# Optimization experiments

Measured on AMD Instinct MI355X. Metric: run time of the kernel, lower is better.

Reference implementation:

```python
import jax, jax.numpy as jnp
import numpy as np

N = 50000      # nodes
E = 800000     # edges
F_IN = 5       # (E, X, Y, Z, T_rel)
D = 128        # hidden_dim
H = 4          # heads
C = D // H     # per-head channels = 32
L = 3          # num_gat_layers
NEG_SLOPE = 0.2


def setup_inputs() -> dict:
    key = jax.random.key(0)
    ks = jax.random.split(key, 20)
    s = 0.05
    inp = {
        "x": jax.random.normal(ks[0], (N, F_IN), dtype=jnp.float32),
        "edge_index": jax.random.randint(ks[1], (2, E), 0, N, dtype=jnp.int32),
        # node encoder
        "enc_W": jax.random.normal(ks[2], (F_IN, D), dtype=jnp.float32) * s,
        "enc_b": jnp.zeros((D,), jnp.float32),
        # stacked GATv2 params for L layers
        "Wl": jax.random.normal(ks[3], (L, D, D), dtype=jnp.float32) * s,
        "bl": jnp.zeros((L, D), jnp.float32),
        "Wr": jax.random.normal(ks[4], (L, D, D), dtype=jnp.float32) * s,
        "br": jnp.zeros((L, D), jnp.float32),
        "att": jax.random.normal(ks[5], (L, H, C), dtype=jnp.float32) * s,
        "gat_bias": jnp.zeros((L, D), jnp.float32),
        # edge classifier MLP (258 -> 128 -> 64 -> 1)
        "c1_W": jax.random.normal(ks[6], (2 * D + 2, D), dtype=jnp.float32) * s,
        "c1_b": jnp.zeros((D,), jnp.float32),
        "c2_W": jax.random.normal(ks[7], (D, 64), dtype=jnp.float32) * s,
        "c2_b": jnp.zeros((64,), jnp.float32),
        "c3_W": jax.random.normal(ks[8], (64, 1), dtype=jnp.float32) * s,
        "c3_b": jnp.zeros((1,), jnp.float32),
    }
    return inp


def _gatv2_layer(h, src, dst, Wl, bl, Wr, br, att, bias):
    # GATv2Conv (PyG semantics, share_weights=False, concat=True, self-loops added)
    xl = (h @ Wl + bl).reshape(N, H, C)   # source transform
    xr = (h @ Wr + br).reshape(N, H, C)   # target transform
    e = jax.nn.leaky_relu(xl[src] + xr[dst], NEG_SLOPE)      # [E', H, C]
    alpha = jnp.einsum("ehc,hc->eh", e, att)                 # [E', H]
    # scatter-softmax over incoming edges of each dst node (numerically stable)
    amax = jax.ops.segment_max(alpha, dst, num_segments=N)
    alpha = jnp.exp(alpha - amax[dst])
    denom = jax.ops.segment_sum(alpha, dst, num_segments=N)
    alpha = alpha / (denom[dst] + 1e-16)
    msg = xl[src] * alpha[:, :, None]                        # [E', H, C]
    out = jax.ops.segment_sum(msg, dst, num_segments=N)      # [N, H, C]
    return out.reshape(N, D) + bias


def reference(x, edge_index, enc_W, enc_b, Wl, bl, Wr, br, att, gat_bias,
              c1_W, c1_b, c2_W, c2_b, c3_W, c3_b):
    h = jax.nn.relu(x @ enc_W + enc_b)
    # add self-loops (PyG GATv2Conv default add_self_loops=True)
    loops = jnp.arange(N, dtype=edge_index.dtype)
    src = jnp.concatenate([edge_index[0], loops])
    dst = jnp.concatenate([edge_index[1], loops])
    for i in range(L):
        h = jax.nn.elu(_gatv2_layer(h, src, dst, Wl[i], bl[i], Wr[i], br[i], att[i], gat_bias[i]))
    # edge feature head on ORIGINAL edges
    row, col = edge_index[0], edge_index[1]
    ni = h[row]                                              # [E, D]
    nj = h[col]                                              # [E, D]
    delta_t = jnp.abs(x[row, 4] - x[col, 4])[:, None]        # [E, 1]
    dist = jnp.sqrt(jnp.sum((x[row, 1:4] - x[col, 1:4]) ** 2, axis=1))[:, None]
    ef = jnp.concatenate([ni, nj, delta_t, dist], axis=1)    # [E, 2D+2]
    o = jax.nn.relu(ef @ c1_W + c1_b)
    o = jax.nn.relu(o @ c2_W + c2_b)
    o = o @ c3_W + c3_b
    return o.reshape(-1)
```

## Files before the change

kernel.cpp:

```cpp
#include <hip/hip_runtime.h>
#include <hip/hip_bf16.h>

#define N_NODES 50000
#define N_EDGES 800000
#define DIM 128
#define NLAYER 3
#define NEG 0.2f

typedef __attribute__((ext_vector_type(8))) short short8;
typedef __attribute__((ext_vector_type(4))) float f32x4;

__global__ __launch_bounds__(256) void zero_kernel(int* p, int n) {
    int i = blockIdx.x * 256 + threadIdx.x;
    if (i < n) p[i] = 0;
}

__global__ __launch_bounds__(256) void hist_kernel(const int* __restrict__ dst, int* __restrict__ counts) {
    int e = blockIdx.x * 256 + threadIdx.x;
    if (e < N_EDGES) atomicAdd(&counts[dst[e]], 1);
}

__global__ __launch_bounds__(256) void scan1_kernel(const int* __restrict__ counts, int* __restrict__ indptr,
                                                    int* __restrict__ bsum, int n) {
    __shared__ int buf[256];
    int t = threadIdx.x;
    int i = blockIdx.x * 256 + t;
    int v = (i < n) ? counts[i] : 0;
    buf[t] = v;
    __syncthreads();
    for (int off = 1; off < 256; off <<= 1) {
        int add = (t >= off) ? buf[t - off] : 0;
        __syncthreads();
        buf[t] += add;
        __syncthreads();
    }
    if (i < n) indptr[i + 1] = buf[t];
    if (t == 255) bsum[blockIdx.x] = buf[255];
}

__global__ __launch_bounds__(256) void scan2_kernel(int* __restrict__ bsum, int* __restrict__ boff,
                                                    int* __restrict__ indptr, int nb) {
    __shared__ int buf[256];
    int t = threadIdx.x;
    int v = (t < nb) ? bsum[t] : 0;
    buf[t] = v;
    __syncthreads();
    for (int off = 1; off < 256; off <<= 1) {
        int add = (t >= off) ? buf[t - off] : 0;
        __syncthreads();
        buf[t] += add;
        __syncthreads();
    }
    if (t < nb) boff[t] = buf[t] - v;
    if (t == 0) indptr[0] = 0;
}

__global__ __launch_bounds__(256) void scan3_kernel(int* __restrict__ indptr, const int* __restrict__ boff, int n) {
    int i = blockIdx.x * 256 + threadIdx.x;
    if (i < n) indptr[i + 1] += boff[i >> 8];
}

__global__ __launch_bounds__(256) void place_kernel(const int* __restrict__ srcp, const int* __restrict__ dstp,
                                                    const int* __restrict__ indptr, int* __restrict__ cursor,
                                                    int* __restrict__ csr_src, int* __restrict__ csr_dst,
                                                    int* __restrict__ csr_eid) {
    int e = blockIdx.x * 256 + threadIdx.x;
    if (e < N_EDGES) {
        int dn = dstp[e];
        int pos = indptr[dn] + atomicAdd(&cursor[dn], 1);
        csr_src[pos] = srcp[e];
        csr_dst[pos] = dn;
        csr_eid[pos] = e;
    }
}

__global__ __launch_bounds__(256) void encoder_kernel(const float* __restrict__ x, const float* __restrict__ W,
                                                      const float* __restrict__ b, float* __restrict__ h) {
    int gid = blockIdx.x * 256 + threadIdx.x;
    int n = gid >> 7, d = gid & 127;
    if (n >= N_NODES) return;
    float acc = b[d];
#pragma unroll
    for (int f = 0; f < 5; f++) acc += x[n * 5 + f] * W[f * DIM + d];
    h[n * DIM + d] = fmaxf(acc, 0.f);
}

__global__ __launch_bounds__(256) void prep_weights_kernel(const float* __restrict__ Wl, const float* __restrict__ Wr,
                                                           const float* __restrict__ c1W,
                                                           unsigned short* __restrict__ wt) {
    int idx = blockIdx.x * 256 + threadIdx.x;
    int m = idx >> 14;
    int r = idx & 16383;
    int n = r >> 7, k = r & 127;
    int L = m >> 1, half = m & 1;
    const float* W;
    if (L < 3) W = (half ? Wr : Wl) + (size_t)L * 16384;
    else W = c1W + (size_t)half * 16384;
    float v = W[k * 128 + n];
    __hip_bfloat16 hb = __float2bfloat16(v);
    float rl = v - __bfloat162float(hb);
    __hip_bfloat16 lb = __float2bfloat16(rl);
    wt[(size_t)m * 32768 + n * 128 + k] = *reinterpret_cast<unsigned short*>(&hb);
    wt[(size_t)m * 32768 + 16384 + n * 128 + k] = *reinterpret_cast<unsigned short*>(&lb);
}

template <bool BF16OUT>
__global__ __launch_bounds__(256) void transform_mfma_kernel(const float* __restrict__ h,
                                                             const unsigned short* __restrict__ wtA,
                                                             const float* __restrict__ bA,
                                                             const unsigned short* __restrict__ wtB,
                                                             const float* __restrict__ bB,
                                                             void* __restrict__ outA_, void* __restrict__ outB_) {
    __shared__ __align__(16) char hhi[64 * 256];
    __shared__ __align__(16) char hlo[64 * 256];
    int t = threadIdx.x;
    int l = t & 63, w = t >> 6;
    int n0 = blockIdx.x * 64;
    for (int i = t; i < 64 * 32; i += 256) {
        int row = i >> 5, c4 = (i & 31) * 4;
        int n = n0 + row;
        float4 v = make_float4(0.f, 0.f, 0.f, 0.f);
        if (n < N_NODES) v = *(const float4*)&h[(size_t)n * DIM + c4];
        const float* pv = &v.x;
        unsigned short hi4[4], lo4[4];
#pragma unroll
        for (int q = 0; q < 4; q++) {
            __hip_bfloat16 hb = __float2bfloat16(pv[q]);
            float rl = pv[q] - __bfloat162float(hb);
            __hip_bfloat16 lb = __float2bfloat16(rl);
            hi4[q] = *reinterpret_cast<unsigned short*>(&hb);
            lo4[q] = *reinterpret_cast<unsigned short*>(&lb);
        }
        int addr = (row * 256 + c4 * 2) ^ ((row & 7) << 4);
        *(ushort4*)(hhi + addr) = make_ushort4(hi4[0], hi4[1], hi4[2], hi4[3]);
        *(ushort4*)(hlo + addr) = make_ushort4(lo4[0], lo4[1], lo4[2], lo4[3]);
    }
    __syncthreads();

    int lane_m = l & 15, lane_k8 = l >> 4;

#pragma unroll
    for (int mat = 0; mat < 2; mat++) {
        const short* wthi = (const short*)(mat ? wtB : wtA);
        const short* wtlo = wthi + 16384;
        const float* bias = mat ? bB : bA;
        short8 bh[2][4], bl_[2][4];
#pragma unroll
        for (int j = 0; j < 2; j++) {
            int nrow = (w * 2 + j) * 16 + lane_m;
#pragma unroll
            for (int ks = 0; ks < 4; ks++) {
                int ke = ks * 32 + lane_k8 * 8;
                bh[j][ks] = *(const short8*)(wthi + nrow * 128 + ke);
                bl_[j][ks] = *(const short8*)(wtlo + nrow * 128 + ke);
            }
        }
        f32x4 acc[4][2];
#pragma unroll
        for (int mt = 0; mt < 4; mt++)
#pragma unroll
            for (int j = 0; j < 2; j++) acc[mt][j] = (f32x4){0.f, 0.f, 0.f, 0.f};
#pragma unroll
        for (int ks = 0; ks < 4; ks++) {
            int kb = ks * 64 + lane_k8 * 16;
#pragma unroll
            for (int mt = 0; mt < 4; mt++) {
                int arow = mt * 16 + lane_m;
                int aswz = (arow & 7) << 4;
                short8 ahi = *(const short8*)(hhi + ((arow * 256 + kb) ^ aswz));
                short8 alo = *(const short8*)(hlo + ((arow * 256 + kb) ^ aswz));
#pragma unroll
                for (int j = 0; j < 2; j++) {
                    acc[mt][j] = __builtin_amdgcn_mfma_f32_16x16x32_bf16(ahi, bh[j][ks], acc[mt][j], 0, 0, 0);
                    acc[mt][j] = __builtin_amdgcn_mfma_f32_16x16x32_bf16(ahi, bl_[j][ks], acc[mt][j], 0, 0, 0);
                    acc[mt][j] = __builtin_amdgcn_mfma_f32_16x16x32_bf16(alo, bh[j][ks], acc[mt][j], 0, 0, 0);
                }
            }
        }
        void* outp = mat ? outB_ : outA_;
#pragma unroll
        for (int j = 0; j < 2; j++) {
            int col = (w * 2 + j) * 16 + lane_m;
            float bv = bias ? bias[col] : 0.f;
#pragma unroll
            for (int mt = 0; mt < 4; mt++) {
#pragma unroll
                for (int r = 0; r < 4; r++) {
                    int node = n0 + mt * 16 + lane_k8 * 4 + r;
                    if (node < N_NODES) {
                        float v = acc[mt][j][r] + bv;
                        if constexpr (BF16OUT) {
                            ((__hip_bfloat16*)outp)[(size_t)node * DIM + col] = __float2bfloat16(v);
                        } else {
                            ((float*)outp)[(size_t)node * DIM + col] = v;
                        }
                    }
                }
            }
        }
    }
}

__global__ __launch_bounds__(256) void gat_edge_kernel(const float* __restrict__ xl, const float* __restrict__ xr,
                                                       const float* __restrict__ att, const float* __restrict__ gbias,
                                                       const int* __restrict__ indptr, const int* __restrict__ csr_src,
                                                       float* __restrict__ h_out) {
    int n = blockIdx.x * 4 + (threadIdx.x >> 6);
    int l = threadIdx.x & 63;
    int half = l >> 5;
    int c0 = (l & 31) * 4;
    float4 xrv = *(const float4*)&xr[(size_t)n * DIM + c0];
    float4 attv = *(const float4*)&att[c0];
    int beg = indptr[n], end = indptr[n + 1];

    float m[4], den[4];
    float4 acc[4];
    {
        float4 v = *(const float4*)&xl[(size_t)n * DIM + c0];
        float z, a;
        z = v.x + xrv.x; z = fmaxf(z, NEG * z); a = z * attv.x;
        z = v.y + xrv.y; z = fmaxf(z, NEG * z); a += z * attv.y;
        z = v.z + xrv.z; z = fmaxf(z, NEG * z); a += z * attv.z;
        z = v.w + xrv.w; z = fmaxf(z, NEG * z); a += z * attv.w;
        a += __shfl_xor(a, 1);
        a += __shfl_xor(a, 2);
        a += __shfl_xor(a, 4);
        if (half == 0) {
            m[0] = a; den[0] = 1.f; acc[0] = v;
        } else {
            m[0] = -3.4e38f; den[0] = 0.f; acc[0] = make_float4(0.f, 0.f, 0.f, 0.f);
        }
#pragma unroll
        for (int c = 1; c < 4; c++) { m[c] = -3.4e38f; den[c] = 0.f; acc[c] = make_float4(0.f, 0.f, 0.f, 0.f); }
    }

    for (int i = beg; i < end; i += 8) {
        int s[4];
        bool val[4];
        float4 v[4];
        float a[4];
#pragma unroll
        for (int c = 0; c < 4; c++) {
            int idx = i + 2 * c + half;
            val[c] = idx < end;
            s[c] = val[c] ? csr_src[idx] : n;
        }
#pragma unroll
        for (int c = 0; c < 4; c++) v[c] = *(const float4*)&xl[(size_t)s[c] * DIM + c0];
#pragma unroll
        for (int c = 0; c < 4; c++) {
            float z, aa;
            z = v[c].x + xrv.x; z = fmaxf(z, NEG * z); aa = z * attv.x;
            z = v[c].y + xrv.y; z = fmaxf(z, NEG * z); aa += z * attv.y;
            z = v[c].z + xrv.z; z = fmaxf(z, NEG * z); aa += z * attv.z;
            z = v[c].w + xrv.w; z = fmaxf(z, NEG * z); aa += z * attv.w;
            a[c] = aa;
        }
#pragma unroll
        for (int off = 1; off <= 4; off <<= 1)
#pragma unroll
            for (int c = 0; c < 4; c++) a[c] += __shfl_xor(a[c], off);
#pragma unroll
        for (int c = 0; c < 4; c++) {
            if (!val[c]) a[c] = -3.4e38f;
            float mn = fmaxf(m[c], a[c]);
            float sc = __expf(m[c] - mn), p = __expf(a[c] - mn);
            den[c] = den[c] * sc + p;
            acc[c].x = acc[c].x * sc + p * v[c].x;
            acc[c].y = acc[c].y * sc + p * v[c].y;
            acc[c].z = acc[c].z * sc + p * v[c].z;
            acc[c].w = acc[c].w * sc + p * v[c].w;
            m[c] = mn;
        }
    }
#pragma unroll
    for (int c = 1; c < 4; c++) {
        float mm = fmaxf(m[0], m[c]);
        float s0 = __expf(m[0] - mm), s1 = __expf(m[c] - mm);
        den[0] = den[0] * s0 + den[c] * s1;
        acc[0].x = acc[0].x * s0 + acc[c].x * s1;
        acc[0].y = acc[0].y * s0 + acc[c].y * s1;
        acc[0].z = acc[0].z * s0 + acc[c].z * s1;
        acc[0].w = acc[0].w * s0 + acc[c].w * s1;
        m[0] = mm;
    }
    {
        float mo = __shfl_xor(m[0], 32);
        float dno = __shfl_xor(den[0], 32);
        float4 ao;
        ao.x = __shfl_xor(acc[0].x, 32);
        ao.y = __shfl_xor(acc[0].y, 32);
        ao.z = __shfl_xor(acc[0].z, 32);
        ao.w = __shfl_xor(acc[0].w, 32);
        float mm = fmaxf(m[0], mo);
        float s0 = __expf(m[0] - mm), s1 = __expf(mo - mm);
        den[0] = den[0] * s0 + dno * s1;
        acc[0].x = acc[0].x * s0 + ao.x * s1;
        acc[0].y = acc[0].y * s0 + ao.y * s1;
        acc[0].z = acc[0].z * s0 + ao.z * s1;
        acc[0].w = acc[0].w * s0 + ao.w * s1;
    }
    if (half == 0) {
        float4 gb = *(const float4*)&gbias[c0];
        float inv = 1.f / (den[0] + 1e-16f);
        float4 o;
        o.x = acc[0].x * inv + gb.x;
        o.y = acc[0].y * inv + gb.y;
        o.z = acc[0].z * inv + gb.z;
        o.w = acc[0].w * inv + gb.w;
        o.x = (o.x > 0.f) ? o.x : __expf(o.x) - 1.f;
        o.y = (o.y > 0.f) ? o.y : __expf(o.y) - 1.f;
        o.z = (o.z > 0.f) ? o.z : __expf(o.z) - 1.f;
        o.w = (o.w > 0.f) ? o.w : __expf(o.w) - 1.f;
        *(float4*)&h_out[(size_t)n * DIM + c0] = o;
    }
}

__global__ __launch_bounds__(256) void edge_mlp_kernel(const unsigned* __restrict__ g1u, const unsigned* __restrict__ g2u,
                                                       const float* __restrict__ x,
                                                       const int* __restrict__ csr_src, const int* __restrict__ csr_dst,
                                                       const int* __restrict__ csr_eid,
                                                       const float* __restrict__ W1tail,
                                                       const float* __restrict__ W2, const float* __restrict__ b2,
                                                       const float* __restrict__ W3, const float* __restrict__ b3,
                                                       float* __restrict__ out, int ntiles) {
    __shared__ __align__(16) char smO1[64 * 256];
    __shared__ __align__(16) char smW2T[64 * 256];
    __shared__ float smCw[2][128];
    __shared__ float smPart[4][64];
    __shared__ int rowi[64], coli[64], seid[64];
    __shared__ float sdt[64], sdi[64];
    int t = threadIdx.x;
    int l = t & 63, w = t >> 6;

    for (int idx = t; idx < 128 * 64; idx += 256) {
        int k = idx >> 6, n = idx & 63;
        __hip_bfloat16 bv = __float2bfloat16(W2[idx]);
        unsigned short us = *reinterpret_cast<unsigned short*>(&bv);
        int addr = (n * 256 + k * 2) ^ ((n & 7) << 4);
        *(unsigned short*)(smW2T + addr) = us;
    }
    if (t < 128) {
        smCw[0][t] = W1tail[t];
        smCw[1][t] = W1tail[128 + t];
    }
    float b3v = b3[0];
    float b2v = b2[w * 16 + (l & 15)];
    float w3v = W3[w * 16 + (l & 15)];
    int koff = (l >> 4) * 16;

    const uint4* g1t = (const uint4*)g1u;
    const uint4* g2t = (const uint4*)g2u;

    for (int tile = blockIdx.x; tile < ntiles; tile += gridDim.x) {
        int p0 = tile * 64;
        __syncthreads();
        if (t < 64) {
            int p = p0 + t;
            int r = csr_src[p], c = csr_dst[p];
            rowi[t] = r; coli[t] = c; seid[t] = csr_eid[p];
            sdt[t] = fabsf(x[r * 5 + 4] - x[c * 5 + 4]);
            float dx = x[r * 5 + 1] - x[c * 5 + 1];
            float dy = x[r * 5 + 2] - x[c * 5 + 2];
            float dz = x[r * 5 + 3] - x[c * 5 + 3];
            sdi[t] = sqrtf(dx * dx + dy * dy + dz * dz);
        }
        __syncthreads();
        for (int idx = t; idx < 64 * 16; idx += 256) {
            int e = idx >> 4, s4 = idx & 15;
            uint4 u1 = g1t[(size_t)rowi[e] * 16 + s4];
            uint4 u2 = g2t[(size_t)coli[e] * 16 + s4];
            float dtv = sdt[e], div = sdi[e];
            unsigned uo[4];
            const unsigned* a1 = &u1.x;
            const unsigned* a2 = &u2.x;
#pragma unroll
            for (int q = 0; q < 4; q++) {
                int d = s4 * 8 + q * 2;
                float lo = __uint_as_float(a1[q] << 16) + __uint_as_float(a2[q] << 16) + dtv * smCw[0][d] + div * smCw[1][d];
                float hi = __uint_as_float(a1[q] & 0xffff0000u) + __uint_as_float(a2[q] & 0xffff0000u) +
                           dtv * smCw[0][d + 1] + div * smCw[1][d + 1];
                lo = fmaxf(lo, 0.f); hi = fmaxf(hi, 0.f);
                __hip_bfloat16 blo = __float2bfloat16(lo), bhi = __float2bfloat16(hi);
                unsigned short ulo = *reinterpret_cast<unsigned short*>(&blo);
                unsigned short uhi = *reinterpret_cast<unsigned short*>(&bhi);
                uo[q] = (unsigned)ulo | ((unsigned)uhi << 16);
            }
            int addr = (e * 256 + s4 * 16) ^ ((e & 7) << 4);
            *(uint4*)(smO1 + addr) = *(uint4*)uo;
        }
        __syncthreads();
        f32x4 acc[4];
#pragma unroll
        for (int mt = 0; mt < 4; mt++) acc[mt] = (f32x4){0.f, 0.f, 0.f, 0.f};
        int nrow = w * 16 + (l & 15);
#pragma unroll
        for (int ks = 0; ks < 4; ks++) {
            short8 bfrag = *(const short8*)(smW2T + ((nrow * 256 + koff + ks * 64) ^ ((nrow & 7) << 4)));
#pragma unroll
            for (int mt = 0; mt < 4; mt++) {
                int mrow = mt * 16 + (l & 15);
                short8 afrag = *(const short8*)(smO1 + ((mrow * 256 + koff + ks * 64) ^ ((mrow & 7) << 4)));
                acc[mt] = __builtin_amdgcn_mfma_f32_16x16x32_bf16(afrag, bfrag, acc[mt], 0, 0, 0);
            }
        }
        float p[4][4];
#pragma unroll
        for (int mt = 0; mt < 4; mt++)
#pragma unroll
            for (int r = 0; r < 4; r++) p[mt][r] = fmaxf(acc[mt][r] + b2v, 0.f) * w3v;
#pragma unroll
        for (int off = 8; off >= 1; off >>= 1)
#pragma unroll
            for (int mt = 0; mt < 4; mt++)
#pragma unroll
                for (int r = 0; r < 4; r++) p[mt][r] += __shfl_xor(p[mt][r], off);
        if ((l & 15) == 0) {
            int g = l >> 4;
#pragma unroll
            for (int mt = 0; mt < 4; mt++)
#pragma unroll
                for (int r = 0; r < 4; r++) smPart[w][mt * 16 + g * 4 + r] = p[mt][r];
        }
        __syncthreads();
        if (t < 64) out[seid[t]] = smPart[0][t] + smPart[1][t] + smPart[2][t] + smPart[3][t] + b3v;
    }
}

extern "C" void kernel_launch(void* const* d_in, const int* in_sizes, int n_in,
                              void* d_out, int out_size, void* d_ws, size_t ws_size,
                              hipStream_t stream) {
    const float* x = (const float*)d_in[0];
    const int* ei = (const int*)d_in[1];
    const float* enc_W = (const float*)d_in[2];
    const float* enc_b = (const float*)d_in[3];
    const float* Wl = (const float*)d_in[4];
    const float* bl = (const float*)d_in[5];
    const float* Wr = (const float*)d_in[6];
    const float* br = (const float*)d_in[7];
    const float* att = (const float*)d_in[8];
    const float* gbias = (const float*)d_in[9];
    const float* c1_W = (const float*)d_in[10];
    const float* c1_b = (const float*)d_in[11];
    const float* c2_W = (const float*)d_in[12];
    const float* c2_b = (const float*)d_in[13];
    const float* c3_W = (const float*)d_in[14];
    const float* c3_b = (const float*)d_in[15];
    float* out = (float*)d_out;

    float* h = (float*)d_ws;
    float* xl = h + (size_t)N_NODES * DIM;
    float* xr = xl + (size_t)N_NODES * DIM;
    int* csr_src = (int*)(xr + (size_t)N_NODES * DIM);
    int* csr_dst = csr_src + N_EDGES;
    int* csr_eid = csr_dst + N_EDGES;
    int* indptr = csr_eid + N_EDGES;
    int* counts = indptr + (N_NODES + 1);
    int* bsum = counts + N_NODES;
    int* boff = bsum + 256;
    uintptr_t wp = (uintptr_t)(boff + 256);
    wp = (wp + 15) & ~(uintptr_t)15;
    unsigned short* wt = (unsigned short*)wp;

    const int* srcp = ei;
    const int* dstp = ei + N_EDGES;
    const int NB = (N_NODES + 255) / 256;
    const int TGRID = (N_NODES + 63) / 64;

    prep_weights_kernel<<<8 * 16384 / 256, 256, 0, stream>>>(Wl, Wr, c1_W, wt);

    zero_kernel<<<(N_NODES + 255) / 256, 256, 0, stream>>>(counts, N_NODES);
    hist_kernel<<<N_EDGES / 256, 256, 0, stream>>>(dstp, counts);
    scan1_kernel<<<NB, 256, 0, stream>>>(counts, indptr, bsum, N_NODES);
    scan2_kernel<<<1, 256, 0, stream>>>(bsum, boff, indptr, NB);
    scan3_kernel<<<NB, 256, 0, stream>>>(indptr, boff, N_NODES);
    zero_kernel<<<(N_NODES + 255) / 256, 256, 0, stream>>>(counts, N_NODES);
    place_kernel<<<N_EDGES / 256, 256, 0, stream>>>(srcp, dstp, indptr, counts, csr_src, csr_dst, csr_eid);

    encoder_kernel<<<(N_NODES * DIM) / 256, 256, 0, stream>>>(x, enc_W, enc_b, h);

    for (int i = 0; i < NLAYER; i++) {
        transform_mfma_kernel<false><<<TGRID, 256, 0, stream>>>(
            h, wt + (size_t)(i * 2) * 32768, bl + (size_t)i * DIM,
            wt + (size_t)(i * 2 + 1) * 32768, br + (size_t)i * DIM, xl, xr);
        gat_edge_kernel<<<N_NODES / 4, 256, 0, stream>>>(xl, xr, att + (size_t)i * DIM,
                                                         gbias + (size_t)i * DIM, indptr, csr_src, h);
    }

    transform_mfma_kernel<true><<<TGRID, 256, 0, stream>>>(
        h, wt + (size_t)6 * 32768, c1_b, wt + (size_t)7 * 32768, nullptr, xl, xr);

    edge_mlp_kernel<<<1024, 256, 0, stream>>>((const unsigned*)xl, (const unsigned*)xr, x,
                                              csr_src, csr_dst, csr_eid, c1_W + 256 * DIM,
                                              c2_W, c2_b, c3_W, c3_b, out, N_EDGES / 64);
}
```

Baseline: 558.1 us.

## Store source-side GAT features in bf16 and split W2 into hi/lo bf16 pair

```diff
diff --git a/kernel.cpp b/kernel.cpp
--- a/kernel.cpp
+++ b/kernel.cpp
@@ -104,7 +104,7 @@
     wt[(size_t)m * 32768 + 16384 + n * 128 + k] = *reinterpret_cast<unsigned short*>(&lb);
 }
 
-template <bool BF16OUT>
+template <bool BF16A, bool BF16B>
 __global__ __launch_bounds__(256) void transform_mfma_kernel(const float* __restrict__ h,
                                                              const unsigned short* __restrict__ wtA,
                                                              const float* __restrict__ bA,
@@ -144,6 +144,7 @@
         const short* wthi = (const short*)(mat ? wtB : wtA);
         const short* wtlo = wthi + 16384;
         const float* bias = mat ? bB : bA;
+        const bool bfout = mat ? BF16B : BF16A;
         short8 bh[2][4], bl_[2][4];
 #pragma unroll
         for (int j = 0; j < 2; j++) {
@@ -189,7 +190,7 @@
                     int node = n0 + mt * 16 + lane_k8 * 4 + r;
                     if (node < N_NODES) {
                         float v = acc[mt][j][r] + bv;
-                        if constexpr (BF16OUT) {
+                        if (bfout) {
                             ((__hip_bfloat16*)outp)[(size_t)node * DIM + col] = __float2bfloat16(v);
                         } else {
                             ((float*)outp)[(size_t)node * DIM + col] = v;
@@ -201,7 +202,17 @@
     }
 }
 
-__global__ __launch_bounds__(256) void gat_edge_kernel(const float* __restrict__ xl, const float* __restrict__ xr,
+__device__ __forceinline__ float4 bf4_to_f4(ushort4 u) {
+    float4 v;
+    v.x = __uint_as_float((unsigned)u.x << 16);
+    v.y = __uint_as_float((unsigned)u.y << 16);
+    v.z = __uint_as_float((unsigned)u.z << 16);
+    v.w = __uint_as_float((unsigned)u.w << 16);
+    return v;
+}
+
+__global__ __launch_bounds__(256) void gat_edge_kernel(const unsigned short* __restrict__ xl,
+                                                       const float* __restrict__ xr,
                                                        const float* __restrict__ att, const float* __restrict__ gbias,
                                                        const int* __restrict__ indptr, const int* __restrict__ csr_src,
                                                        float* __restrict__ h_out) {
@@ -216,7 +227,7 @@
     float m[4], den[4];
     float4 acc[4];
     {
-        float4 v = *(const float4*)&xl[(size_t)n * DIM + c0];
+        float4 v = bf4_to_f4(*(const ushort4*)&xl[(size_t)n * DIM + c0]);
         float z, a;
         z = v.x + xrv.x; z = fmaxf(z, NEG * z); a = z * attv.x;
         z = v.y + xrv.y; z = fmaxf(z, NEG * z); a += z * attv.y;
@@ -246,7 +257,7 @@
             s[c] = val[c] ? csr_src[idx] : n;
         }
 #pragma unroll
-        for (int c = 0; c < 4; c++) v[c] = *(const float4*)&xl[(size_t)s[c] * DIM + c0];
+        for (int c = 0; c < 4; c++) v[c] = bf4_to_f4(*(const ushort4*)&xl[(size_t)s[c] * DIM + c0]);
 #pragma unroll
         for (int c = 0; c < 4; c++) {
             float z, aa;
@@ -326,6 +337,7 @@
                                                        float* __restrict__ out, int ntiles) {
     __shared__ __align__(16) char smO1[64 * 256];
     __shared__ __align__(16) char smW2T[64 * 256];
+    __shared__ __align__(16) char smW2Tlo[64 * 256];
     __shared__ float smCw[2][128];
     __shared__ float smPart[4][64];
     __shared__ int rowi[64], coli[64], seid[64];
@@ -335,10 +347,13 @@
 
     for (int idx = t; idx < 128 * 64; idx += 256) {
         int k = idx >> 6, n = idx & 63;
-        __hip_bfloat16 bv = __float2bfloat16(W2[idx]);
-        unsigned short us = *reinterpret_cast<unsigned short*>(&bv);
+        float v = W2[idx];
+        __hip_bfloat16 hb = __float2bfloat16(v);
+        float rl = v - __bfloat162float(hb);
+        __hip_bfloat16 lb = __float2bfloat16(rl);
         int addr = (n * 256 + k * 2) ^ ((n & 7) << 4);
-        *(unsigned short*)(smW2T + addr) = us;
+        *(unsigned short*)(smW2T + addr) = *reinterpret_cast<unsigned short*>(&hb);
+        *(unsigned short*)(smW2Tlo + addr) = *reinterpret_cast<unsigned short*>(&lb);
     }
     if (t < 128) {
         smCw[0][t] = W1tail[t];
@@ -396,12 +411,15 @@
         int nrow = w * 16 + (l & 15);
 #pragma unroll
         for (int ks = 0; ks < 4; ks++) {
-            short8 bfrag = *(const short8*)(smW2T + ((nrow * 256 + koff + ks * 64) ^ ((nrow & 7) << 4)));
+            int baddr = (nrow * 256 + koff + ks * 64) ^ ((nrow & 7) << 4);
+            short8 bhi = *(const short8*)(smW2T + baddr);
+            short8 blo = *(const short8*)(smW2Tlo + baddr);
 #pragma unroll
             for (int mt = 0; mt < 4; mt++) {
                 int mrow = mt * 16 + (l & 15);
                 short8 afrag = *(const short8*)(smO1 + ((mrow * 256 + koff + ks * 64) ^ ((mrow & 7) << 4)));
-                acc[mt] = __builtin_amdgcn_mfma_f32_16x16x32_bf16(afrag, bfrag, acc[mt], 0, 0, 0);
+                acc[mt] = __builtin_amdgcn_mfma_f32_16x16x32_bf16(afrag, bhi, acc[mt], 0, 0, 0);
+                acc[mt] = __builtin_amdgcn_mfma_f32_16x16x32_bf16(afrag, blo, acc[mt], 0, 0, 0);
             }
         }
         float p[4][4];
@@ -480,14 +498,15 @@
     encoder_kernel<<<(N_NODES * DIM) / 256, 256, 0, stream>>>(x, enc_W, enc_b, h);
 
     for (int i = 0; i < NLAYER; i++) {
-        transform_mfma_kernel<false><<<TGRID, 256, 0, stream>>>(
+        transform_mfma_kernel<true, false><<<TGRID, 256, 0, stream>>>(
             h, wt + (size_t)(i * 2) * 32768, bl + (size_t)i * DIM,
             wt + (size_t)(i * 2 + 1) * 32768, br + (size_t)i * DIM, xl, xr);
-        gat_edge_kernel<<<N_NODES / 4, 256, 0, stream>>>(xl, xr, att + (size_t)i * DIM,
+        gat_edge_kernel<<<N_NODES / 4, 256, 0, stream>>>((const unsigned short*)xl, xr,
+                                                         att + (size_t)i * DIM,
                                                          gbias + (size_t)i * DIM, indptr, csr_src, h);
     }
 
-    transform_mfma_kernel<true><<<TGRID, 256, 0, stream>>>(
+    transform_mfma_kernel<true, true><<<TGRID, 256, 0, stream>>>(
         h, wt + (size_t)6 * 32768, c1_b, wt + (size_t)7 * 32768, nullptr, xl, xr);
 
     edge_mlp_kernel<<<1024, 256, 0, stream>>>((const unsigned*)xl, (const unsigned*)xr, x,
```

After: 558.7 us. Within noise of the previous version (+0.1%).
